# Optimization experiments

Measured on AMD Instinct MI355X. Metric: run time of the kernel, lower is better.

## Reference

```python
import jax, jax.numpy as jnp
import numpy as np
from jax import lax

B, L, D = 2, 1024, 1024
EXPAND, N, K = 2, 16, 4          # expand, d_state, d_conv
DI = EXPAND * D                  # d_inner = 2048
R = (D + 15) // 16               # dt_rank = 64
EPS = 1e-5


def setup_inputs() -> dict:
    key = jax.random.key(0)
    ks = jax.random.split(key, 8)
    x = jax.random.normal(ks[0], (B, L, D), dtype=jnp.float32)
    ln_w = jnp.ones((D,), jnp.float32)
    ln_b = jnp.zeros((D,), jnp.float32)
    W_in = jax.random.normal(ks[1], (D, 2 * DI), jnp.float32) * (1.0 / np.sqrt(D))
    conv_w = jax.random.normal(ks[2], (DI, K), jnp.float32) * 0.2
    conv_b = jnp.zeros((DI,), jnp.float32)
    W_x = jax.random.normal(ks[3], (DI, R + 2 * N), jnp.float32) * (1.0 / np.sqrt(DI))
    W_dt = jax.random.normal(ks[4], (R, DI), jnp.float32) * (1.0 / np.sqrt(R))
    b_dt = jnp.full((DI,), -4.0, jnp.float32)  # softplus(-4) ~ 0.018 dt init
    A_log = jnp.log(jnp.broadcast_to(jnp.arange(1, N + 1, dtype=jnp.float32), (DI, N)))
    D_param = jnp.ones((DI,), jnp.float32)
    W_out = jax.random.normal(ks[5], (DI, D), jnp.float32) * (1.0 / np.sqrt(DI))
    return {"x": x, "ln_w": ln_w, "ln_b": ln_b, "W_in": W_in, "conv_w": conv_w,
            "conv_b": conv_b, "W_x": W_x, "W_dt": W_dt, "b_dt": b_dt,
            "A_log": A_log, "D_param": D_param, "W_out": W_out}


def _mamba_block(x, ln_w, ln_b, W_in, conv_w, conv_b, W_x, W_dt, b_dt, A_log, D_param, W_out):
    # pre-LayerNorm
    mu = jnp.mean(x, axis=-1, keepdims=True)
    xc = x - mu
    var = jnp.mean(xc * xc, axis=-1, keepdims=True)
    h = xc * lax.rsqrt(var + EPS) * ln_w + ln_b          # [B,L,D]

    xz = h @ W_in                                        # [B,L,2*DI]
    xi, z = xz[..., :DI], xz[..., DI:]

    # depthwise causal conv1d, kernel K, left pad K-1
    xp = jnp.pad(xi, ((0, 0), (K - 1, 0), (0, 0)))
    conv = conv_b
    for k in range(K):
        conv = conv + xp[:, k:k + L, :] * conv_w[:, k]
    u = jax.nn.silu(conv)                                # [B,L,DI]

    proj = u @ W_x                                       # [B,L,R+2N]
    dt_r = proj[..., :R]
    Bm = proj[..., R:R + N]                              # [B,L,N]
    Cm = proj[..., R + N:]                               # [B,L,N]
    dt = jax.nn.softplus(dt_r @ W_dt + b_dt)             # [B,L,DI]

    A = -jnp.exp(A_log)                                  # [DI,N]
    dA = jnp.exp(dt[..., None] * A)                      # [B,L,DI,N]
    dBu = (dt * u)[..., None] * Bm[:, :, None, :]        # [B,L,DI,N]

    def comb(e1, e2):
        a1, b1 = e1
        a2, b2 = e2
        return a1 * a2, a2 * b1 + b2

    _, hs = lax.associative_scan(comb, (dA, dBu), axis=1)  # [B,L,DI,N]
    y = jnp.einsum('bldn,bln->bld', hs, Cm) + u * D_param
    y = y * jax.nn.silu(z)
    return x + y @ W_out


def reference(x, ln_w, ln_b, W_in, conv_w, conv_b, W_x, W_dt, b_dt, A_log, D_param, W_out):
    return _mamba_block(x, ln_w, ln_b, W_in, conv_w, conv_b, W_x, W_dt, b_dt,
                        A_log, D_param, W_out)
```

## Files before the change

### kernel.cpp

```cpp
#include <hip/hip_runtime.h>
#include <hip/hip_bf16.h>
#include <math.h>

#define B_ 2
#define L_ 1024
#define D_ 1024
#define DI_ 2048
#define K_ 4
#define N_ 16
#define R_ 64
#define BL_ (B_ * L_)
#define EPS_ 1e-5f

#define IDX4(l) ((l) + (((l) >> 6) << 2))

typedef __attribute__((ext_vector_type(8))) short short8;
typedef __attribute__((ext_vector_type(4))) float f32x4;

__device__ inline unsigned short f2bf(float f) {
    unsigned u = __float_as_uint(f);
    unsigned r = (u + 0x7fffu + ((u >> 16) & 1u)) >> 16;
    return (unsigned short)r;
}
__device__ inline float bf2f(unsigned short s) {
    return __uint_as_float(((unsigned)s) << 16);
}
__device__ inline float fast_silu(float z) {
    return z * __builtin_amdgcn_rcpf(1.f + __expf(-z));
}
#if __has_builtin(__builtin_amdgcn_exp2f)
__device__ inline float fexp2(float x) { return __builtin_amdgcn_exp2f(x); }
#else
__device__ inline float fexp2(float x) { return exp2f(x); }
#endif
__device__ inline void gl_lds16(const void* g, void* l) {
    __builtin_amdgcn_global_load_lds(
        (const __attribute__((address_space(1))) void*)g,
        (__attribute__((address_space(3))) void*)l, 16, 0, 0);
}

template <int CTRL>
__device__ inline float dpp_shr(float x) {
    return __int_as_float(__builtin_amdgcn_update_dpp(
        0, __float_as_int(x), CTRL, 0xf, 0xf, true));
}
__device__ inline float row16_sum(float p) {
    p += dpp_shr<0x111>(p);
    p += dpp_shr<0x112>(p);
    p += dpp_shr<0x114>(p);
    p += dpp_shr<0x118>(p);
    return p;
}

__global__ void ln_kernel(const float* __restrict__ x, const float* __restrict__ w,
                          const float* __restrict__ b, unsigned short* __restrict__ hb) {
    int row = blockIdx.x;
    const float* xr = x + (size_t)row * D_;
    float4 v = ((const float4*)xr)[threadIdx.x];

    __shared__ float red[4];
    float s = v.x + v.y + v.z + v.w;
    for (int off = 1; off < 64; off <<= 1) s += __shfl_xor(s, off, 64);
    if ((threadIdx.x & 63) == 0) red[threadIdx.x >> 6] = s;
    __syncthreads();
    float mu = (red[0] + red[1] + red[2] + red[3]) * (1.0f / D_);
    __syncthreads();
    float cx = v.x - mu, cy = v.y - mu, cz = v.z - mu, cw = v.w - mu;
    float sq = cx*cx + cy*cy + cz*cz + cw*cw;
    for (int off = 1; off < 64; off <<= 1) sq += __shfl_xor(sq, off, 64);
    if ((threadIdx.x & 63) == 0) red[threadIdx.x >> 6] = sq;
    __syncthreads();
    float var = (red[0] + red[1] + red[2] + red[3]) * (1.0f / D_);
    float rstd = rsqrtf(var + EPS_);

    float4 wv = ((const float4*)w)[threadIdx.x];
    float4 bv = ((const float4*)b)[threadIdx.x];
    ushort4 o;
    o.x = f2bf(cx * rstd * wv.x + bv.x);
    o.y = f2bf(cy * rstd * wv.y + bv.y);
    o.z = f2bf(cz * rstd * wv.z + bv.z);
    o.w = f2bf(cw * rstd * wv.w + bv.w);
    ((ushort4*)(hb + (size_t)row * D_))[threadIdx.x] = o;
}

__global__ void transpose_cast_all(const float* __restrict__ W_in, const float* __restrict__ W_x,
                                   const float* __restrict__ W_out,
                                   unsigned short* __restrict__ WinT, unsigned short* __restrict__ WxT,
                                   unsigned short* __restrict__ WoutT) {
    int bid = blockIdx.x;
    const float* W; unsigned short* WT; int K, N, bx, by;
    if (bid < 4096)      { W = W_in;  WT = WinT;  K = 1024; N = 4096; bx = bid & 127; by = bid >> 7; }
    else if (bid < 4288) { int id = bid - 4096; W = W_x;  WT = WxT;  K = DI_; N = 96;   bx = id % 3;  by = id / 3; }
    else                 { int id = bid - 4288; W = W_out; WT = WoutT; K = DI_; N = 1024; bx = id & 31; by = id >> 5; }
    __shared__ float tile[32][33];
    int k0 = by * 32, n0 = bx * 32;
    int tr = threadIdx.x >> 5;
    int tc = threadIdx.x & 31;
#pragma unroll
    for (int i = 0; i < 4; ++i)
        tile[tr + i*8][tc] = W[(size_t)(k0 + tr + i*8) * N + n0 + tc];
    __syncthreads();
#pragma unroll
    for (int i = 0; i < 4; ++i)
        WT[(size_t)(n0 + tr + i*8) * K + k0 + tc] = f2bf(tile[tc][tr + i*8]);
}

template <int BN, int MODE>
__global__ __launch_bounds__(256) void mfma_gemm_bt(
        const unsigned short* __restrict__ A,  int lda,
        const unsigned short* __restrict__ BT, int ldb,
        float* __restrict__ C, int ldc, int Kchunk,
        float* __restrict__ xi, unsigned short* __restrict__ sz) {
    constexpr int NT = BN / 32;
    __shared__ unsigned short As[128 * 32];
    __shared__ unsigned short Bs[BN * 32];

    int tid = threadIdx.x;
    int wave = tid >> 6, lane = tid & 63;
    int lane15 = lane & 15, quad = lane >> 4;
    int wr = wave >> 1, wc = wave & 1;

    int m0 = blockIdx.y * 128;
    int n0 = blockIdx.x * BN;
    int kbeg = blockIdx.z * Kchunk;
    int kend = kbeg + Kchunk;

    f32x4 acc[4][NT];
#pragma unroll
    for (int i = 0; i < 4; ++i)
#pragma unroll
        for (int j = 0; j < NT; ++j) acc[i][j] = (f32x4){0.f, 0.f, 0.f, 0.f};

    constexpr int ACALLS = 8;
    constexpr int BCALLS = BN * 4 / 64;

    for (int k0 = kbeg; k0 < kend; k0 += 32) {
        __syncthreads();
        for (int c = wave; c < ACALLS + BCALLS; c += 4) {
            if (c < ACALLS) {
                int cell = c * 64 + lane;
                int m = cell >> 2, s = cell & 3;
                int q = s ^ (m & 3) ^ ((m >> 2) & 3);
                gl_lds16(A + (size_t)(m0 + m) * lda + k0 + q * 8, &As[c * 512]);
            } else {
                int cell = (c - ACALLS) * 64 + lane;
                int n = cell >> 2, s = cell & 3;
                int q = s ^ (n & 3) ^ ((n >> 2) & 3);
                gl_lds16(BT + (size_t)(n0 + n) * ldb + k0 + q * 8, &Bs[(c - ACALLS) * 512]);
            }
        }
        __syncthreads();

        short8 af[4], bfr[NT];
#pragma unroll
        for (int i = 0; i < 4; ++i) {
            int m = wr * 64 + i * 16 + lane15;
            int s = quad ^ (m & 3) ^ ((m >> 2) & 3);
            af[i] = *(const short8*)&As[m * 32 + s * 8];
        }
#pragma unroll
        for (int j = 0; j < NT; ++j) {
            int n = wc * (NT * 16) + j * 16 + lane15;
            int s = quad ^ (n & 3) ^ ((n >> 2) & 3);
            bfr[j] = *(const short8*)&Bs[n * 32 + s * 8];
        }
#pragma unroll
        for (int i = 0; i < 4; ++i)
#pragma unroll
            for (int j = 0; j < NT; ++j)
                acc[i][j] = __builtin_amdgcn_mfma_f32_16x16x32_bf16(af[i], bfr[j], acc[i][j], 0, 0, 0);
    }

#pragma unroll
    for (int i = 0; i < 4; ++i) {
        int row = m0 + wr * 64 + i * 16 + quad * 4;
#pragma unroll
        for (int j = 0; j < NT; ++j) {
            int col = n0 + wc * (NT * 16) + j * 16 + lane15;
#pragma unroll
            for (int r = 0; r < 4; ++r) {
                float v = acc[i][j][r];
                int rr = row + r;
                if (MODE == 0) {
                    C[(size_t)rr * ldc + col] = v;
                } else if (MODE == 1) {
                    atomicAdd(&C[(size_t)rr * ldc + col], v);
                } else {
                    if (col < DI_) xi[(size_t)rr * DI_ + col] = v;
                    else           sz[(size_t)rr * DI_ + (col - DI_)] = f2bf(fast_silu(v));
                }
            }
        }
    }
}

__global__ void conv_silu_kernel(const float* __restrict__ xi, const float* __restrict__ cw,
                                 const float* __restrict__ cb, unsigned short* __restrict__ ub) {
    int idx = blockIdx.x * blockDim.x + threadIdx.x;
    int c = idx & (DI_ - 1);
    int bl = idx >> 11;
    int l = bl & (L_ - 1);
    float4 w4 = ((const float4*)cw)[c];
    float acc = cb[c];
    const float* base = xi + (size_t)bl * DI_ + c;
    if (l >= 3) {
        acc = fmaf(base[-(size_t)3 * DI_], w4.x, acc);
        acc = fmaf(base[-(size_t)2 * DI_], w4.y, acc);
        acc = fmaf(base[-(size_t)1 * DI_], w4.z, acc);
        acc = fmaf(base[0],                w4.w, acc);
    } else {
        if (l >= 2) acc = fmaf(*(base - 2 * DI_), w4.y, acc);
        if (l >= 1) acc = fmaf(*(base - 1 * DI_), w4.z, acc);
        acc = fmaf(base[0], w4.w, acc);
    }
    ub[idx] = f2bf(fast_silu(acc));
}

__global__ __launch_bounds__(256) void dtprep(
        const float* __restrict__ proj, const float* __restrict__ W_dt,
        const float* __restrict__ b_dt, const unsigned short* __restrict__ ub,
        const unsigned short* __restrict__ szb, const float* __restrict__ Dp,
        float2* __restrict__ dtduT, unsigned int* __restrict__ szdT) {
    __shared__ alignas(16) unsigned char smem[64 * 65 * 8];
    float (*As)[68] = reinterpret_cast<float(*)[68]>(smem);
    float (*Bs)[64] = reinterpret_cast<float(*)[64]>(smem + 4352);
    float2 (*T2)[65] = reinterpret_cast<float2(*)[65]>(smem);
    unsigned int (*TU)[65] = reinterpret_cast<unsigned int(*)[65]>(smem);

    int tid = threadIdx.x;
    int n0 = blockIdx.x * 64;
    int m0 = blockIdx.y * 64;
    int ar = tid >> 2, ak = (tid & 3) << 2;
    int kb = tid >> 4, bc = (tid & 15) << 2;
    int ty = tid >> 4, tx = tid & 15;

    float acc[4][4] = {};
#pragma unroll
    for (int k0 = 0; k0 < R_; k0 += 16) {
        float4 av = *(const float4*)&proj[(size_t)(m0 + ar) * 96 + k0 + ak];
        As[ak + 0][ar] = av.x; As[ak + 1][ar] = av.y;
        As[ak + 2][ar] = av.z; As[ak + 3][ar] = av.w;
        float4 bv = *(const float4*)&W_dt[(size_t)(k0 + kb) * DI_ + n0 + bc];
        Bs[kb][bc + 0] = bv.x; Bs[kb][bc + 1] = bv.y;
        Bs[kb][bc + 2] = bv.z; Bs[kb][bc + 3] = bv.w;
        __syncthreads();
#pragma unroll
        for (int kk = 0; kk < 16; ++kk) {
            float a[4], bb[4];
#pragma unroll
            for (int i = 0; i < 4; ++i) a[i] = As[kk][ty * 4 + i];
#pragma unroll
            for (int j = 0; j < 4; ++j) bb[j] = Bs[kk][tx * 4 + j];
#pragma unroll
            for (int i = 0; i < 4; ++i)
#pragma unroll
                for (int j = 0; j < 4; ++j)
                    acc[i][j] = fmaf(a[i], bb[j], acc[i][j]);
        }
        __syncthreads();
    }

    float4 bd = *(const float4*)&b_dt[n0 + tx * 4];
    float4 dp4 = *(const float4*)&Dp[n0 + tx * 4];
    float bda[4] = {bd.x, bd.y, bd.z, bd.w};
    float dpa[4] = {dp4.x, dp4.y, dp4.z, dp4.w};
    float2 d2[4][4];
    unsigned int su[4][4];
#pragma unroll
    for (int i = 0; i < 4; ++i) {
        int bl = m0 + ty * 4 + i;
        ushort4 u4 = *(const ushort4*)&ub[(size_t)bl * DI_ + n0 + tx * 4];
        ushort4 s4 = *(const ushort4*)&szb[(size_t)bl * DI_ + n0 + tx * 4];
        unsigned short ua[4] = {u4.x, u4.y, u4.z, u4.w};
        unsigned short sa[4] = {s4.x, s4.y, s4.z, s4.w};
#pragma unroll
        for (int j = 0; j < 4; ++j) {
            float v = acc[i][j] + bda[j];
            float dtv = fmaxf(v, 0.f) + __logf(1.f + __expf(-fabsf(v)));
            float uu = bf2f(ua[j]);
            float szv = bf2f(sa[j]);
            d2[i][j] = make_float2(dtv, dtv * uu);
            su[i][j] = ((unsigned)f2bf(uu * dpa[j] * szv) << 16) | (unsigned)f2bf(szv);
        }
    }

#pragma unroll
    for (int i = 0; i < 4; ++i)
#pragma unroll
        for (int j = 0; j < 4; ++j)
            T2[ty * 4 + i][tx * 4 + j] = d2[i][j];
    __syncthreads();
#pragma unroll
    for (int i = 0; i < 8; ++i) {
        int c_l = (tid >> 5) + i * 8;
#pragma unroll
        for (int jj = 0; jj < 2; ++jj) {
            int bl_l = (tid & 31) + jj * 32;
            dtduT[(size_t)(n0 + c_l) * BL_ + m0 + bl_l] = T2[bl_l][c_l];
        }
    }
    __syncthreads();

#pragma unroll
    for (int i = 0; i < 4; ++i)
#pragma unroll
        for (int j = 0; j < 4; ++j)
            TU[ty * 4 + i][tx * 4 + j] = su[i][j];
    __syncthreads();
#pragma unroll
    for (int i = 0; i < 8; ++i) {
        int c_l = (tid >> 5) + i * 8;
#pragma unroll
        for (int jj = 0; jj < 2; ++jj) {
            int bl_l = (tid & 31) + jj * 32;
            szdT[(size_t)(n0 + c_l) * BL_ + m0 + bl_l] = TU[bl_l][c_l];
        }
    }
}

__global__ __launch_bounds__(256, 8) void scan_v7(
        const float2* __restrict__ dtduT, const unsigned int* __restrict__ szdT,
        const float* __restrict__ proj, const float* __restrict__ A_log,
        unsigned short* __restrict__ yzT) {
    int bc = blockIdx.x;
    int b = bc >> 10;
    int cp = bc & 1023;
    int t = threadIdx.x;
    int n = t & 15;
    int cs = (t >> 4) & 1;
    int chunk = t >> 5;
    int c = cp * 2 + cs;

    __shared__ float sA[8][32];
    __shared__ float sB[8][32];
    __shared__ float ps[2][L_ + 64];

    float A2 = -__expf(A_log[c * N_ + n]) * 1.4426950408889634f;
    int l0 = chunk * 128;
    const float* pB = proj + (size_t)b * L_ * 96 + R_ + n;
    const float* pC = pB + N_;
    const float4* gd = (const float4*)(dtduT + (size_t)c * BL_ + (size_t)b * L_);

    float a = 1.f, acc = 0.f;
#pragma unroll
    for (int h = 0; h < 2; ++h) {
        int lb = l0 + h * 64;
        const float4* gdd = gd + (lb >> 1);
        const float* pBb = pB + (size_t)lb * 96;
#pragma unroll
        for (int q = 0; q < 16; ++q) {
            float4 d0 = gdd[q * 2];
            float4 d1 = gdd[q * 2 + 1];
            float b0 = pBb[(q*4 + 0) * 96];
            float b1 = pBb[(q*4 + 1) * 96];
            float b2 = pBb[(q*4 + 2) * 96];
            float b3 = pBb[(q*4 + 3) * 96];
            float e;
            e = fexp2(d0.x * A2); a *= e; acc = fmaf(e, acc, d0.y * b0);
            e = fexp2(d0.z * A2); a *= e; acc = fmaf(e, acc, d0.w * b1);
            e = fexp2(d1.x * A2); a *= e; acc = fmaf(e, acc, d1.y * b2);
            e = fexp2(d1.z * A2); a *= e; acc = fmaf(e, acc, d1.w * b3);
        }
    }
    sA[chunk][t & 31] = a;
    sB[chunk][t & 31] = acc;
    __syncthreads();

    if (t < 32) {
        float hc = 0.f;
#pragma unroll
        for (int j = 0; j < 8; ++j) {
            float aj = sA[j][t];
            float bj = sB[j][t];
            sB[j][t] = hc;
            hc = fmaf(aj, hc, bj);
        }
    }
    __syncthreads();
    float h = sB[chunk][t & 31];

#pragma unroll
    for (int hh = 0; hh < 2; ++hh) {
        int lb = l0 + hh * 64;
        const float4* gdd = gd + (lb >> 1);
        const float* pBb = pB + (size_t)lb * 96;
        const float* pCb = pC + (size_t)lb * 96;
        float* psb = &ps[cs][IDX4(lb)];
#pragma unroll
        for (int q = 0; q < 16; ++q) {
            float4 d0 = gdd[q * 2];
            float4 d1 = gdd[q * 2 + 1];
            float b0 = pBb[(q*4 + 0) * 96], c0 = pCb[(q*4 + 0) * 96];
            float b1 = pBb[(q*4 + 1) * 96], c1 = pCb[(q*4 + 1) * 96];
            float b2 = pBb[(q*4 + 2) * 96], c2 = pCb[(q*4 + 2) * 96];
            float b3 = pBb[(q*4 + 3) * 96], c3 = pCb[(q*4 + 3) * 96];
            float e, p0, p1, p2, p3;
            e = fexp2(d0.x * A2); h = fmaf(e, h, d0.y * b0); p0 = row16_sum(h * c0);
            e = fexp2(d0.z * A2); h = fmaf(e, h, d0.w * b1); p1 = row16_sum(h * c1);
            e = fexp2(d1.x * A2); h = fmaf(e, h, d1.y * b2); p2 = row16_sum(h * c2);
            e = fexp2(d1.z * A2); h = fmaf(e, h, d1.w * b3); p3 = row16_sum(h * c3);
            if (n == 15) *(float4*)&psb[q * 4] = (float4){p0, p1, p2, p3};
        }
    }
    __syncthreads();

    {
        int half = t >> 7;
        int tt = t & 127;
        int l = tt * 8;
        int c_out = cp * 2 + half;
        size_t tb = (size_t)c_out * BL_ + (size_t)b * L_;
        const float* pp = &ps[half][IDX4(l)];
        ushort4 o[2];
#pragma unroll
        for (int g = 0; g < 2; ++g) {
            float4 p4 = *(const float4*)(pp + g * 4);
            uint4 sd4 = *(const uint4*)(szdT + tb + l + g * 4);
            o[g].x = f2bf(p4.x * bf2f((unsigned short)(sd4.x & 0xffff)) + bf2f((unsigned short)(sd4.x >> 16)));
            o[g].y = f2bf(p4.y * bf2f((unsigned short)(sd4.y & 0xffff)) + bf2f((unsigned short)(sd4.y >> 16)));
            o[g].z = f2bf(p4.z * bf2f((unsigned short)(sd4.z & 0xffff)) + bf2f((unsigned short)(sd4.z >> 16)));
            o[g].w = f2bf(p4.w * bf2f((unsigned short)(sd4.w & 0xffff)) + bf2f((unsigned short)(sd4.w >> 16)));
        }
        *(ushort4*)(yzT + tb + l) = o[0];
        *(ushort4*)(yzT + tb + l + 4) = o[1];
    }
}

__global__ void transpose_y(const unsigned short* __restrict__ yzT, unsigned short* __restrict__ yz) {
    __shared__ unsigned short t[32][33];
    int c0 = blockIdx.y * 32, bl0 = blockIdx.x * 32;
    int r = threadIdx.x >> 5;
    int col = threadIdx.x & 31;
#pragma unroll
    for (int i = 0; i < 4; ++i)
        t[r + i*8][col] = yzT[(size_t)(c0 + r + i*8) * BL_ + bl0 + col];
    __syncthreads();
#pragma unroll
    for (int i = 0; i < 4; ++i)
        yz[(size_t)(bl0 + r + i*8) * DI_ + c0 + col] = t[col][r + i*8];
}

extern "C" void kernel_launch(void* const* d_in, const int* in_sizes, int n_in,
                              void* d_out, int out_size, void* d_ws, size_t ws_size,
                              hipStream_t stream) {
    const float* x       = (const float*)d_in[0];
    const float* ln_w    = (const float*)d_in[1];
    const float* ln_b    = (const float*)d_in[2];
    const float* W_in    = (const float*)d_in[3];
    const float* conv_w  = (const float*)d_in[4];
    const float* conv_b  = (const float*)d_in[5];
    const float* W_x     = (const float*)d_in[6];
    const float* W_dt    = (const float*)d_in[7];
    const float* b_dt    = (const float*)d_in[8];
    const float* A_log   = (const float*)d_in[9];
    const float* D_param = (const float*)d_in[10];
    const float* W_out   = (const float*)d_in[11];
    float* out = (float*)d_out;

    uint8_t* p = (uint8_t*)d_ws;
    unsigned short* hb    = (unsigned short*)p;  p += (size_t)BL_ * D_ * 2;
    unsigned short* WinT  = (unsigned short*)p;  p += (size_t)4096 * 1024 * 2;
    float*          xib   = (float*)p;           p += (size_t)BL_ * DI_ * 4;
    unsigned short* szb   = (unsigned short*)p;  p += (size_t)BL_ * DI_ * 2;
    unsigned short* ub    = (unsigned short*)p;  p += (size_t)BL_ * DI_ * 2;
    unsigned short* WxT   = (unsigned short*)p;  p += (size_t)96 * DI_ * 2;
    float*          proj  = (float*)p;           p += (size_t)BL_ * 96 * 4;
    unsigned short* WoutT = (unsigned short*)p;  p += (size_t)1024 * DI_ * 2;
    float2*         dtduT = (float2*)p;          p += (size_t)BL_ * DI_ * 8;
    unsigned int*   szdT  = (unsigned int*)p;    p += (size_t)BL_ * DI_ * 4;
    unsigned short* yzT   = (unsigned short*)p;  p += (size_t)BL_ * DI_ * 2;
    unsigned short* yzb   = (unsigned short*)d_ws;

    hipMemsetAsync(proj, 0, (size_t)BL_ * 96 * 4, stream);
    hipMemcpyAsync(out, x, (size_t)BL_ * D_ * 4, hipMemcpyDeviceToDevice, stream);

    transpose_cast_all<<<6336, 256, 0, stream>>>(W_in, W_x, W_out, WinT, WxT, WoutT);

    ln_kernel<<<BL_, 256, 0, stream>>>(x, ln_w, ln_b, hb);

    mfma_gemm_bt<128, 3><<<dim3(4096 / 128, BL_ / 128, 1), 256, 0, stream>>>(
        hb, 1024, WinT, 1024, nullptr, 0, 1024, xib, szb);

    conv_silu_kernel<<<(BL_ * DI_) / 256, 256, 0, stream>>>(xib, conv_w, conv_b, ub);

    mfma_gemm_bt<96, 1><<<dim3(1, BL_ / 128, 16), 256, 0, stream>>>(
        ub, DI_, WxT, DI_, proj, 96, 128, nullptr, nullptr);

    dtprep<<<dim3(DI_ / 64, BL_ / 64), 256, 0, stream>>>(
        proj, W_dt, b_dt, ub, szb, D_param, dtduT, szdT);

    scan_v7<<<B_ * DI_ / 2, 256, 0, stream>>>(dtduT, szdT, proj, A_log, yzT);

    transpose_y<<<dim3(BL_ / 32, DI_ / 32), 256, 0, stream>>>(yzT, yzb);

    mfma_gemm_bt<128, 1><<<dim3(1024 / 128, BL_ / 128, 2), 256, 0, stream>>>(
        yzb, DI_, WoutT, DI_, out, 1024, 1024, nullptr, nullptr);
}
```

Baseline: 300.2 us.

## Split scan into 16 shorter chunks with 512 threads and stage dt/du in LDS

The selective-scan kernel now runs 512 threads per block, so each thread walks a 64-step chunk instead of a 128-step chunk. The sequential dependency per thread is halved, and the inter-chunk carry pass grows from 8 to 16 steps. The dt/du pairs are cooperatively loaded once into padded shared memory rather than read twice from global memory across the two passes. In exchange the kernel uses more LDS and has tighter register limits under the 512-thread launch bound, which could reduce occupancy.

After: 281.1 us. -6.4%, faster.

```diff
diff --git a/kernel.cpp b/kernel.cpp
--- a/kernel.cpp
+++ b/kernel.cpp
@@ -318,7 +318,7 @@
     }
 }
 
-__global__ __launch_bounds__(256, 8) void scan_v7(
+__global__ __launch_bounds__(512, 8) void scan_v8(
         const float2* __restrict__ dtduT, const unsigned int* __restrict__ szdT,
         const float* __restrict__ proj, const float* __restrict__ A_log,
         unsigned short* __restrict__ yzT) {
@@ -331,45 +331,53 @@
     int chunk = t >> 5;
     int c = cp * 2 + cs;
 
-    __shared__ float sA[8][32];
-    __shared__ float sB[8][32];
-    __shared__ float ps[2][L_ + 64];
+    __shared__ float dd[2][2120];
+    __shared__ float sA[16][32];
+    __shared__ float sB[16][32];
+    __shared__ float ps[2][1096];
+
+    {
+        int half = t >> 8;
+        int tt = t & 255;
+        int l = tt * 4;
+        int cload = cp * 2 + half;
+        const float4* g = (const float4*)(dtduT + (size_t)cload * BL_ + (size_t)b * L_ + l);
+        int il2 = l + ((l >> 6) << 1);
+        float* dst = &dd[half][il2 * 2];
+        *(float4*)(dst + 0) = g[0];
+        *(float4*)(dst + 4) = g[1];
+    }
+    __syncthreads();
 
     float A2 = -__expf(A_log[c * N_ + n]) * 1.4426950408889634f;
-    int l0 = chunk * 128;
-    const float* pB = proj + (size_t)b * L_ * 96 + R_ + n;
+    int lb = chunk * 64;
+    const float* ddp = &dd[cs][(lb + ((lb >> 6) << 1)) * 2];
+    const float* pB = proj + (size_t)b * L_ * 96 + R_ + n + (size_t)lb * 96;
     const float* pC = pB + N_;
-    const float4* gd = (const float4*)(dtduT + (size_t)c * BL_ + (size_t)b * L_);
 
     float a = 1.f, acc = 0.f;
 #pragma unroll
-    for (int h = 0; h < 2; ++h) {
-        int lb = l0 + h * 64;
-        const float4* gdd = gd + (lb >> 1);
-        const float* pBb = pB + (size_t)lb * 96;
-#pragma unroll
-        for (int q = 0; q < 16; ++q) {
-            float4 d0 = gdd[q * 2];
-            float4 d1 = gdd[q * 2 + 1];
-            float b0 = pBb[(q*4 + 0) * 96];
-            float b1 = pBb[(q*4 + 1) * 96];
-            float b2 = pBb[(q*4 + 2) * 96];
-            float b3 = pBb[(q*4 + 3) * 96];
-            float e;
-            e = fexp2(d0.x * A2); a *= e; acc = fmaf(e, acc, d0.y * b0);
-            e = fexp2(d0.z * A2); a *= e; acc = fmaf(e, acc, d0.w * b1);
-            e = fexp2(d1.x * A2); a *= e; acc = fmaf(e, acc, d1.y * b2);
-            e = fexp2(d1.z * A2); a *= e; acc = fmaf(e, acc, d1.w * b3);
-        }
-    }
-    sA[chunk][t & 31] = a;
-    sB[chunk][t & 31] = acc;
+    for (int q = 0; q < 16; ++q) {
+        float4 d0 = *(const float4*)(ddp + q * 8);
+        float4 d1 = *(const float4*)(ddp + q * 8 + 4);
+        float b0 = pB[(q*4 + 0) * 96];
+        float b1 = pB[(q*4 + 1) * 96];
+        float b2 = pB[(q*4 + 2) * 96];
+        float b3 = pB[(q*4 + 3) * 96];
+        float e;
+        e = fexp2(d0.x * A2); a *= e; acc = fmaf(e, acc, d0.y * b0);
+        e = fexp2(d0.z * A2); a *= e; acc = fmaf(e, acc, d0.w * b1);
+        e = fexp2(d1.x * A2); a *= e; acc = fmaf(e, acc, d1.y * b2);
+        e = fexp2(d1.z * A2); a *= e; acc = fmaf(e, acc, d1.w * b3);
+    }
+    sA[chunk][cs * 16 + n] = a;
+    sB[chunk][cs * 16 + n] = acc;
     __syncthreads();
 
     if (t < 32) {
         float hc = 0.f;
 #pragma unroll
-        for (int j = 0; j < 8; ++j) {
+        for (int j = 0; j < 16; ++j) {
             float aj = sA[j][t];
             float bj = sB[j][t];
             sB[j][t] = hc;
@@ -377,52 +385,41 @@
         }
     }
     __syncthreads();
-    float h = sB[chunk][t & 31];
-
-#pragma unroll
-    for (int hh = 0; hh < 2; ++hh) {
-        int lb = l0 + hh * 64;
-        const float4* gdd = gd + (lb >> 1);
-        const float* pBb = pB + (size_t)lb * 96;
-        const float* pCb = pC + (size_t)lb * 96;
-        float* psb = &ps[cs][IDX4(lb)];
-#pragma unroll
-        for (int q = 0; q < 16; ++q) {
-            float4 d0 = gdd[q * 2];
-            float4 d1 = gdd[q * 2 + 1];
-            float b0 = pBb[(q*4 + 0) * 96], c0 = pCb[(q*4 + 0) * 96];
-            float b1 = pBb[(q*4 + 1) * 96], c1 = pCb[(q*4 + 1) * 96];
-            float b2 = pBb[(q*4 + 2) * 96], c2 = pCb[(q*4 + 2) * 96];
-            float b3 = pBb[(q*4 + 3) * 96], c3 = pCb[(q*4 + 3) * 96];
-            float e, p0, p1, p2, p3;
-            e = fexp2(d0.x * A2); h = fmaf(e, h, d0.y * b0); p0 = row16_sum(h * c0);
-            e = fexp2(d0.z * A2); h = fmaf(e, h, d0.w * b1); p1 = row16_sum(h * c1);
-            e = fexp2(d1.x * A2); h = fmaf(e, h, d1.y * b2); p2 = row16_sum(h * c2);
-            e = fexp2(d1.z * A2); h = fmaf(e, h, d1.w * b3); p3 = row16_sum(h * c3);
-            if (n == 15) *(float4*)&psb[q * 4] = (float4){p0, p1, p2, p3};
-        }
+    float h = sB[chunk][cs * 16 + n];
+
+    float* psb = &ps[cs][IDX4(lb)];
+#pragma unroll
+    for (int q = 0; q < 16; ++q) {
+        float4 d0 = *(const float4*)(ddp + q * 8);
+        float4 d1 = *(const float4*)(ddp + q * 8 + 4);
+        float b0 = pB[(q*4 + 0) * 96], c0 = pC[(q*4 + 0) * 96];
+        float b1 = pB[(q*4 + 1) * 96], c1 = pC[(q*4 + 1) * 96];
+        float b2 = pB[(q*4 + 2) * 96], c2 = pC[(q*4 + 2) * 96];
+        float b3 = pB[(q*4 + 3) * 96], c3 = pC[(q*4 + 3) * 96];
+        float e, p0, p1, p2, p3;
+        e = fexp2(d0.x * A2); h = fmaf(e, h, d0.y * b0); p0 = row16_sum(h * c0);
+        e = fexp2(d0.z * A2); h = fmaf(e, h, d0.w * b1); p1 = row16_sum(h * c1);
+        e = fexp2(d1.x * A2); h = fmaf(e, h, d1.y * b2); p2 = row16_sum(h * c2);
+        e = fexp2(d1.z * A2); h = fmaf(e, h, d1.w * b3); p3 = row16_sum(h * c3);
+        if (n == 15) *(float4*)&psb[q * 4] = (float4){p0, p1, p2, p3};
     }
     __syncthreads();
 
     {
-        int half = t >> 7;
-        int tt = t & 127;
-        int l = tt * 8;
+        int half = t >> 8;
+        int tt = t & 255;
+        int l = tt * 4;
         int c_out = cp * 2 + half;
         size_t tb = (size_t)c_out * BL_ + (size_t)b * L_;
         const float* pp = &ps[half][IDX4(l)];
-        ushort4 o[2];
-#pragma unroll
-        for (int g = 0; g < 2; ++g) {
-            float4 p4 = *(const float4*)(pp + g * 4);
-            uint4 sd4 = *(const uint4*)(szdT + tb + l + g * 4);
-            o[g].x = f2bf(p4.x * bf2f((unsigned short)(sd4.x & 0xffff)) + bf2f((unsigned short)(sd4.x >> 16)));
-            o[g].y = f2bf(p4.y * bf2f((unsigned short)(sd4.y & 0xffff)) + bf2f((unsigned short)(sd4.y >> 16)));
-            o[g].z = f2bf(p4.z * bf2f((unsigned short)(sd4.z & 0xffff)) + bf2f((unsigned short)(sd4.z >> 16)));
-            o[g].w = f2bf(p4.w * bf2f((unsigned short)(sd4.w & 0xffff)) + bf2f((unsigned short)(sd4.w >> 16)));
-        }
-        *(ushort4*)(yzT + tb + l) = o[0];
-        *(ushort4*)(yzT + tb + l + 4) = o[1];
+        float4 p4 = *(const float4*)pp;
+        uint4 sd4 = *(const uint4*)(szdT + tb + l);
+        ushort4 o;
+        o.x = f2bf(p4.x * bf2f((unsigned short)(sd4.x & 0xffff)) + bf2f((unsigned short)(sd4.x >> 16)));
+        o.y = f2bf(p4.y * bf2f((unsigned short)(sd4.y & 0xffff)) + bf2f((unsigned short)(sd4.y >> 16)));
+        o.z = f2bf(p4.z * bf2f((unsigned short)(sd4.z & 0xffff)) + bf2f((unsigned short)(sd4.z >> 16)));
+        o.w = f2bf(p4.w * bf2f((unsigned short)(sd4.w & 0xffff)) + bf2f((unsigned short)(sd4.w >> 16)));
+        *(ushort4*)(yzT + tb + l) = o;
     }
 }
 
@@ -489,7 +486,7 @@
     dtprep<<<dim3(DI_ / 64, BL_ / 64), 256, 0, stream>>>(
         proj, W_dt, b_dt, ub, szb, D_param, dtduT, szdT);
 
-    scan_v7<<<B_ * DI_ / 2, 256, 0, stream>>>(dtduT, szdT, proj, A_log, yzT);
+    scan_v8<<<B_ * DI_ / 2, 512, 0, stream>>>(dtduT, szdT, proj, A_log, yzT);
 
     transpose_y<<<dim3(BL_ / 32, DI_ / 32), 256, 0, stream>>>(yzT, yzb);
 
```
